# Performance work log

Measured on AMD Instinct MI355X. Metric: run time of the kernel, lower is better.

The kernel has to match this reference:

```python
import jax, jax.numpy as jnp
import numpy as np

B, T, N = 16, 1024, 128
WIN, STEP = 30, 2
MOMENT_ORDERS = (2, 4, 8)
D_MODEL = 256


def _mask_diag(corr):
    n = corr.shape[-1]
    eye = jnp.eye(n, dtype=corr.dtype)
    return corr * (1.0 - eye) + eye


def corrcoef_time(xw):
    # xw: [..., L, N] -> corr over channels: [..., N, N]
    L = xw.shape[-2]
    xm = xw - xw.mean(axis=-2, keepdims=True)
    cov = jnp.einsum('...ln,...lm->...nm', xm, xm) / (L - 1 + 1e-8)
    var = jnp.clip(jnp.diagonal(cov, axis1=-2, axis2=-1), 1e-8, None)
    std = jnp.sqrt(var)
    corr = cov / (std[..., :, None] * std[..., None, :])
    corr = jnp.nan_to_num(corr, nan=0.0, posinf=0.0, neginf=0.0)
    return _mask_diag(corr)


def rowwise_corr(M):
    # M: [B, N, F]
    Xc = M - M.mean(axis=-1, keepdims=True)
    num = jnp.einsum('bnf,bmf->bnm', Xc, Xc)
    den1 = jnp.sqrt(jnp.clip((Xc ** 2).sum(axis=-1), 1e-8, None))
    corr = num / (den1[:, :, None] * den1[:, None, :])
    corr = jnp.nan_to_num(corr, nan=0.0, posinf=0.0, neginf=0.0)
    return _mask_diag(corr)


def layer_norm(x, gamma, beta, eps=1e-5):
    mu = x.mean(axis=-1, keepdims=True)
    var = ((x - mu) ** 2).mean(axis=-1, keepdims=True)
    return (x - mu) / jnp.sqrt(var + eps) * gamma + beta


def normalize_adj(adj):
    n = adj.shape[-1]
    A_hat = adj + jnp.eye(n, dtype=adj.dtype)
    d = A_hat.sum(axis=-1)
    dis = jnp.sqrt(1.0 / jnp.clip(d, 1e-8, None))
    return A_hat * dis[:, :, None] * dis[:, None, :]


def setup_inputs() -> dict:
    key = jax.random.key(0)
    ks = jax.random.split(key, 8)
    in_dim = len(MOMENT_ORDERS) * N
    return {
        'x': jax.random.normal(ks[0], (B, T, N), dtype=jnp.float32),
        'ln_gamma': jnp.ones((in_dim,), jnp.float32),
        'ln_beta': jnp.zeros((in_dim,), jnp.float32),
        'W1': jax.random.normal(ks[1], (in_dim, D_MODEL), jnp.float32) * 0.05,
        'b1': jnp.zeros((D_MODEL,), jnp.float32),
        'W2': jax.random.normal(ks[2], (D_MODEL, D_MODEL), jnp.float32) * 0.05,
        'b2': jnp.zeros((D_MODEL,), jnp.float32),
        'Wc': jax.random.normal(ks[3], (D_MODEL, 1), jnp.float32) * 0.05,
        'bc': jnp.zeros((1,), jnp.float32),
    }


def reference(x, ln_gamma, ln_beta, W1, b1, W2, b2, Wc, bc):
    # sliding windows (static indices)
    starts = np.arange(0, T - WIN + 1, STEP)
    idx = starts[:, None] + np.arange(WIN)[None, :]
    xw = x[:, idx, :]
    lo = corrcoef_time(xw)                            # [B, Wn, N, N]

    mean_lo = lo.mean(axis=1, keepdims=True)
    centered = lo - mean_lo
    cm_list, ho_list = [], []
    for d in MOMENT_ORDERS:
        cm = jnp.nan_to_num((centered ** d).mean(axis=1),
                            nan=0.0, posinf=0.0, neginf=0.0)  # [B, N, N]
        cm_list.append(cm)
        ho_list.append(rowwise_corr(cm))

    X = jnp.concatenate(cm_list, axis=-1)             # [B, N, 3N]
    X = layer_norm(X, ln_gamma, ln_beta)

    A = jnp.stack(ho_list, axis=1).mean(axis=1)
    A = 0.5 * (A + jnp.swapaxes(A, 1, 2))
    A_norm = normalize_adj(A)

    H = jax.nn.relu(jnp.einsum('bnm,bmd->bnd', A_norm, X @ W1 + b1))
    H = jax.nn.relu(jnp.einsum('bnm,bmd->bnd', A_norm, H @ W2 + b2))
    g = H.mean(axis=1)                                # [B, d_model]
    out = jax.nn.sigmoid(g @ Wc + bc)                 # [B, 1]
    return out
```

## Files before the change

kernel.cpp:

```cpp
#include <hip/hip_runtime.h>
#include <math.h>

#define BB  16
#define TT  1024
#define NN  128
#define WIN 30
#define NWD 498
#define DM  256
#define IND 384
#define GW  16

#define INV_W (1.0f/498.0f)

#define SARR (BB*NN*NN)

#define OFF_A     0
#define OFF_G     (OFF_A    + BB*NWD*NN)
#define OFF_CM2   (OFF_G    + BB*NWD*NN)
#define OFF_CM4   (OFF_CM2  + SARR)
#define OFF_CM8   (OFF_CM4  + SARR)
#define OFF_AD    (OFF_CM8  + SARR)
#define OFF_PART  (OFF_AD   + 3*SARR)
#define OFF_ANORM OFF_PART
#define OFF_BUFA  (OFF_ANORM + SARR)
#define OFF_BUFB  (OFF_BUFA + BB*NN*DM)
#define OFF_CTR   (OFF_PART + 768*16384)

#define GLL16(gsrc, ldst) \
    __builtin_amdgcn_global_load_lds((const __attribute__((address_space(1))) void*)(gsrc), \
                                     (__attribute__((address_space(3))) void*)(ldst), 16, 0, 0)

__global__ __launch_bounds__(128) void k1_stats(const float* __restrict__ x, float* __restrict__ ws) {
    int bx = blockIdx.x;
    if (bx == 0 && threadIdx.x < 128) ((unsigned*)(ws + OFF_CTR))[threadIdx.x] = 0u;
    int c = bx & 15, b = bx >> 4;
    int w0 = c*32, w1 = min(NWD, w0+32);
    int n = threadIdx.x;
    const float* xp = x + (size_t)b*TT*NN + n;

    float sum = 0.f, sq = 0.f;
    for (int t = 2*w0; t < 2*w0 + WIN; ++t) {
        float v = xp[(size_t)t*NN];
        sum += v; sq = fmaf(v, v, sq);
    }
    for (int w = w0; w < w1; ++w) {
        if (w > w0) {
            float o0 = xp[(size_t)(2*w-2)*NN], o1 = xp[(size_t)(2*w-1)*NN];
            float n0 = xp[(size_t)(2*w+28)*NN], n1 = xp[(size_t)(2*w+29)*NN];
            sum += (n0 + n1) - (o0 + o1);
            sq  += (n0*n0 + n1*n1) - (o0*o0 + o1*o1);
        }
        float mean = sum * (1.0f/30.0f);
        float ss = sq - 30.0f*mean*mean;
        float var = fmaxf(ss * (1.0f/29.0f), 1e-8f);
        float a = (1.0f / sqrtf(var)) * 0.185695338f;
        ws[OFF_A + ((size_t)b*NWD + w)*NN + n] = a;
        ws[OFF_G + ((size_t)b*NWD + w)*NN + n] = mean * a * 5.477225575f;
    }
}

__global__ __launch_bounds__(256) __attribute__((amdgpu_waves_per_eu(3, 3)))
void k24_inc(const float* __restrict__ x, float* __restrict__ ws) {
    __shared__ __align__(16) float xr[64][NN];
    __shared__ __align__(16) float sa[GW][NN];
    __shared__ __align__(16) float sg[GW][NN];
    int bx = blockIdx.x;
    int wc = bx & 7;
    int slab = (bx >> 3) % 6;
    int b = bx / 48;
    const char IS[6] = {0,0,0,0,1,1};
    const char JS[6] = {0,1,2,3,2,3};
    int is = IS[slab], js = JS[slab];
    int w0 = wc * 63, w1 = min(NWD, w0 + 63);
    int tid = threadIdx.x;
    int jg = tid & 7, ig = tid >> 3;
    int i0 = is*64 + ig*2;
    int j0 = js*32 + jg*4;

    const float* xb = x + (size_t)b*TT*NN;
    const float* Ab = ws + OFF_A + (size_t)b*NWD*NN;
    const float* Gb = ws + OFF_G + (size_t)b*NWD*NN;

    float P[2][4];
    float S1[2][4], S2[2][4], S3[2][4], S4[2][4], S5[2][4], S6[2][4], S7[2][4], S8[2][4];
#pragma unroll
    for (int p=0;p<2;++p)
#pragma unroll
        for (int q=0;q<4;++q) {
            P[p][q]=0.f;
            S1[p][q]=0.f;S2[p][q]=0.f;S3[p][q]=0.f;S4[p][q]=0.f;
            S5[p][q]=0.f;S6[p][q]=0.f;S7[p][q]=0.f;S8[p][q]=0.f;
        }

    auto moments = [&](int k) {
        float2 ai = *(const float2*)&sa[k][i0];
        float2 gi = *(const float2*)&sg[k][i0];
        float4 aj = *(const float4*)&sa[k][j0];
        float4 gj = *(const float4*)&sg[k][j0];
        float av[2] = {ai.x, ai.y};
        float mg[2] = {-gi.x, -gi.y};
        float aw[4] = {aj.x, aj.y, aj.z, aj.w};
        float gw[4] = {gj.x, gj.y, gj.z, gj.w};
#pragma unroll
        for (int p=0;p<2;++p)
#pragma unroll
            for (int q=0;q<4;++q) {
                float aa  = av[p]*aw[q];
                float ngg = mg[p]*gw[q];
                float c   = fmaf(P[p][q], aa, ngg);
                float c2 = c*c;
                float c3 = c2*c;
                float c4 = c2*c2;
                S1[p][q] += c;
                S2[p][q] += c2;
                S3[p][q] += c3;
                S4[p][q] += c4;
                S5[p][q] = fmaf(c4, c,  S5[p][q]);
                S6[p][q] = fmaf(c3, c3, S6[p][q]);
                S7[p][q] = fmaf(c3, c4, S7[p][q]);
                S8[p][q] = fmaf(c4, c4, S8[p][q]);
            }
    };

    int rlo = 2*w0;
    for (int wg = w0; wg < w1; wg += GW) {
        int m = min(GW, w1 - wg);
        __syncthreads();
        int rhi = 2*(wg + m - 1) + 29;
        int nr = rhi - rlo + 1;
        for (int idx = tid; idx < nr*32; idx += 256) {
            int r = idx >> 5, c4 = idx & 31;
            int t = rlo + r;
            GLL16(xb + (size_t)t*NN + c4*4, &xr[t & 63][c4*4]);
        }
        for (int idx = tid; idx < m*32; idx += 256) {
            int k = idx >> 5, c4 = idx & 31;
            GLL16(Ab + (size_t)(wg+k)*NN + c4*4, &sa[k][c4*4]);
        }
        for (int idx = tid; idx < m*32; idx += 256) {
            int k = idx >> 5, c4 = idx & 31;
            GLL16(Gb + (size_t)(wg+k)*NN + c4*4, &sg[k][c4*4]);
        }
        rlo = rhi + 1;
        __syncthreads();

        int kstart = 0;
        if (wg == w0) {
#pragma unroll 6
            for (int k = 0; k < WIN; ++k) {
                int t = 2*w0 + k;
                float2 xi = *(const float2*)&xr[t & 63][i0];
                float4 xj = *(const float4*)&xr[t & 63][j0];
                float av[2] = {xi.x, xi.y};
                float bv[4] = {xj.x, xj.y, xj.z, xj.w};
#pragma unroll
                for (int p=0;p<2;++p)
#pragma unroll
                    for (int q=0;q<4;++q) P[p][q] = fmaf(av[p], bv[q], P[p][q]);
            }
            moments(0);
            kstart = 1;
        }
        for (int k = kstart; k < m; ++k) {
            int w = wg + k;
            int tr[4] = {2*w - 2, 2*w - 1, 2*w + 28, 2*w + 29};
#pragma unroll
            for (int kk = 0; kk < 4; ++kk) {
                int t = tr[kk];
                float sgn = (kk < 2) ? -1.0f : 1.0f;
                float2 xi = *(const float2*)&xr[t & 63][i0];
                float4 xj = *(const float4*)&xr[t & 63][j0];
                float av[2] = {sgn*xi.x, sgn*xi.y};
                float bv[4] = {xj.x, xj.y, xj.z, xj.w};
#pragma unroll
                for (int p=0;p<2;++p)
#pragma unroll
                    for (int q=0;q<4;++q) P[p][q] = fmaf(av[p], bv[q], P[p][q]);
            }
            moments(k);
        }
    }

    float* tp = ws + OFF_PART + (size_t)bx*16384 + tid*8;
#define STORE_ARR(A, S) \
    *(float4*)&tp[(A)*2048]     = make_float4(S[0][0], S[0][1], S[0][2], S[0][3]); \
    *(float4*)&tp[(A)*2048 + 4] = make_float4(S[1][0], S[1][1], S[1][2], S[1][3]);
    STORE_ARR(0, S1) STORE_ARR(1, S2) STORE_ARR(2, S3) STORE_ARR(3, S4)
    STORE_ARR(4, S5) STORE_ARR(5, S6) STORE_ARR(6, S7) STORE_ARR(7, S8)
#undef STORE_ARR
}

__global__ __launch_bounds__(256) void kred(float* __restrict__ ws) {
    int pair = blockIdx.x >> 3, sub = blockIdx.x & 7;
    int b = pair / 6, slab = pair % 6;
    const char IS[6] = {0,0,0,0,1,1};
    const char JS[6] = {0,1,2,3,2,3};
    int is = IS[slab], js = JS[slab];
    int off = sub*256 + threadIdx.x;
    const float* base = ws + OFF_PART + (size_t)(b*48 + slab*8)*16384;

    float E[8];
#pragma unroll
    for (int a=0;a<8;++a) E[a] = 0.f;
    for (int c = 0; c < 8; ++c) {
        const float* tp = base + (size_t)c*16384;
#pragma unroll
        for (int a=0;a<8;++a) E[a] += tp[a*2048 + off];
    }

    int tid_old = off >> 3, e = off & 7;
    int ig = tid_old >> 3, jg = tid_old & 7;
    int p = e >> 2, q = e & 3;
    int i = is*64 + ig*2 + p;
    int j = js*32 + jg*4 + q;

    float cm2, cm4, cm8;
    if (i == j) {
        cm2 = 0.f; cm4 = 0.f; cm8 = 0.f;
    } else {
        float e1 = E[0]*INV_W, e2 = E[1]*INV_W, e3 = E[2]*INV_W, e4 = E[3]*INV_W;
        float e5 = E[4]*INV_W, e6 = E[5]*INV_W, e7 = E[6]*INV_W, e8 = E[7]*INV_W;
        float m  = e1;
        float m2 = m*m, m3 = m2*m, m4 = m2*m2, m5 = m4*m, m6 = m3*m3, m8 = m4*m4;
        cm2 = e2 - m2;
        cm4 = e4 - 4.f*m*e3 + 6.f*m2*e2 - 3.f*m4;
        cm8 = e8 - 8.f*m*e7 + 28.f*m2*e6 - 56.f*m3*e5 + 70.f*m4*e4
                 - 56.f*m5*e3 + 28.f*m6*e2 - 7.f*m8;
    }
    float* C2 = ws + OFF_CM2 + (size_t)b*NN*NN;
    float* C4 = ws + OFF_CM4 + (size_t)b*NN*NN;
    float* C8 = ws + OFF_CM8 + (size_t)b*NN*NN;
    C2[i*NN + j] = cm2; C2[j*NN + i] = cm2;
    C4[i*NN + j] = cm4; C4[j*NN + i] = cm4;
    C8[i*NN + j] = cm8; C8[j*NN + i] = cm8;
}

#define XSTR 132
__global__ __launch_bounds__(256) void kB(const float* __restrict__ gamma, const float* __restrict__ beta,
                                          const float* __restrict__ W1, const float* __restrict__ b1,
                                          float* __restrict__ ws) {
    __shared__ __align__(16) float smem[NN*XSTR + 2*NN];
    __shared__ unsigned winB;
    int blk = blockIdx.x, tid = threadIdx.x;
    if (blk < 192) {
        int rem = blk % 12;
        int b = blk / 12, di = rem >> 2, jq = rem & 3;
        float* Xct = smem;
        float* Mr  = smem + NN*XSTR;
        float* Ir  = Mr + NN;
        const float* cm = ws + (di==0 ? OFF_CM2 : (di==1 ? OFF_CM4 : OFF_CM8)) + (size_t)b*NN*NN;
        for (int idx = tid; idx < NN*NN; idx += 256) {
            int n = idx >> 7, f = idx & 127;
            Xct[f*XSTR + n] = cm[idx];
        }
        __syncthreads();
        if (tid < NN) {
            float s1 = 0.f, s2 = 0.f;
            for (int f = 0; f < NN; ++f) { float v = Xct[f*XSTR + tid]; s1 += v; s2 = fmaf(v, v, s2); }
            float mean = s1 * (1.0f/NN);
            Mr[tid] = mean;
            Ir[tid] = 1.0f/sqrtf(fmaxf(s2 - (float)NN*mean*mean, 1e-8f));
        }
        __syncthreads();
        int n0 = (tid >> 4)*8, m0 = jq*32 + (tid & 15)*2;
        float acc0[8], acc1[8];
#pragma unroll
        for (int k=0;k<8;++k) { acc0[k]=0.f; acc1[k]=0.f; }
        for (int f = 0; f < NN; ++f) {
            const float* row = &Xct[f*XSTR];
            float4 a0 = *(const float4*)&row[n0];
            float4 a1 = *(const float4*)&row[n0+4];
            float2 bm = *(const float2*)&row[m0];
            float av[8] = {a0.x,a0.y,a0.z,a0.w,a1.x,a1.y,a1.z,a1.w};
#pragma unroll
            for (int k=0;k<8;++k) {
                acc0[k] = fmaf(av[k], bm.x, acc0[k]);
                acc1[k] = fmaf(av[k], bm.y, acc1[k]);
            }
        }
        float rm0 = Mr[m0], rm1 = Mr[m0+1], im0 = Ir[m0], im1 = Ir[m0+1];
        float* Ad = ws + OFF_AD + (size_t)(b*3 + di)*NN*NN;
#pragma unroll
        for (int k=0;k<8;++k) {
            int gi = n0+k;
            float rn = Mr[gi], inv = Ir[gi];
            float v0 = (acc0[k] - (float)NN*rn*rm0) * inv * im0;
            float v1 = (acc1[k] - (float)NN*rn*rm1) * inv * im1;
            if (gi == m0)   v0 = 1.0f;
            if (gi == m0+1) v1 = 1.0f;
            Ad[gi*NN + m0]     = v0;
            Ad[gi*NN + m0 + 1] = v1;
        }

        __syncthreads();
        if (tid == 0) {
            unsigned* ctr = (unsigned*)(ws + OFF_CTR);
            unsigned old = __hip_atomic_fetch_add(&ctr[96 + b], 1u,
                                                  __ATOMIC_ACQ_REL, __HIP_MEMORY_SCOPE_AGENT);
            winB = (old == 11u) ? 1u : 0u;
        }
        __syncthreads();
        if (winB) {
            float* As = smem;
            float* dis = smem + NN*(NN+1);
            const float* A0 = ws + OFF_AD + (size_t)(b*3 + 0)*NN*NN;
            const float* A1 = ws + OFF_AD + (size_t)(b*3 + 1)*NN*NN;
            const float* A2 = ws + OFF_AD + (size_t)(b*3 + 2)*NN*NN;
            for (int idx = tid; idx < NN*NN; idx += 256) {
                int n = idx >> 7, m = idx & 127;
                int ji = m*NN + n;
                float s = A0[idx] + A0[ji] + A1[idx] + A1[ji] + A2[idx] + A2[ji];
                As[n*(NN+1)+m] = s * (1.0f/6.0f);
            }
            __syncthreads();
            if (tid < NN) {
                float d = 1.0f;
                for (int m = 0; m < NN; ++m) d += As[tid*(NN+1)+m];
                dis[tid] = sqrtf(1.0f / fmaxf(d, 1e-8f));
            }
            __syncthreads();
            float* An = ws + OFF_ANORM + (size_t)b*NN*NN;
            for (int idx = tid; idx < NN*NN; idx += 256) {
                int n = idx >> 7, m = idx & 127;
                float v = As[n*(NN+1)+m] + (n==m ? 1.0f : 0.0f);
                An[idx] = v * dis[n] * dis[m];
            }
        }
    } else {
        int r0 = (blk - 192) * 8;
        float* Xs = smem;
        float* sm = smem + 8*IND;
        float* sr = sm + 8;
        for (int r = 0; r < 8; ++r) {
            int row = r0 + r;
            int b = row >> 7, n = row & 127;
            const float* c2 = ws + OFF_CM2 + ((size_t)b*NN + n)*NN;
            const float* c4 = ws + OFF_CM4 + ((size_t)b*NN + n)*NN;
            const float* c8 = ws + OFF_CM8 + ((size_t)b*NN + n)*NN;
            for (int c = tid; c < IND; c += 256)
                Xs[r*IND+c] = (c < 128) ? c2[c] : (c < 256) ? c4[c-128] : c8[c-256];
        }
        __syncthreads();
        {
            int team = tid >> 5, lane = tid & 31;
            float s = 0.f;
            for (int c = lane; c < IND; c += 32) s += Xs[team*IND + c];
#pragma unroll
            for (int o = 16; o > 0; o >>= 1) s += __shfl_down(s, o, 32);
            float mean = __shfl(s, 0, 32) * (1.0f/IND);
            float v = 0.f;
            for (int c = lane; c < IND; c += 32) { float d = Xs[team*IND + c] - mean; v = fmaf(d, d, v); }
#pragma unroll
            for (int o = 16; o > 0; o >>= 1) v += __shfl_down(v, o, 32);
            if (lane == 0) {
                sm[team] = mean;
                sr[team] = 1.0f / sqrtf(v*(1.0f/IND) + 1e-5f);
            }
        }
        __syncthreads();
        for (int r = 0; r < 8; ++r) {
            float mean = sm[r], rstd = sr[r];
            for (int c = tid; c < IND; c += 256)
                Xs[r*IND+c] = (Xs[r*IND+c] - mean)*rstd*gamma[c] + beta[c];
        }
        __syncthreads();
        float acc[8];
        float bv = b1[tid];
#pragma unroll
        for (int r = 0; r < 8; ++r) acc[r] = bv;
        for (int kk = 0; kk < IND; kk += 4) {
            float w0 = W1[(size_t)(kk+0)*DM + tid];
            float w1 = W1[(size_t)(kk+1)*DM + tid];
            float w2 = W1[(size_t)(kk+2)*DM + tid];
            float w3 = W1[(size_t)(kk+3)*DM + tid];
#pragma unroll
            for (int r = 0; r < 8; ++r) {
                float4 xv = *(const float4*)&Xs[r*IND + kk];
                acc[r] = fmaf(xv.x, w0, acc[r]);
                acc[r] = fmaf(xv.y, w1, acc[r]);
                acc[r] = fmaf(xv.z, w2, acc[r]);
                acc[r] = fmaf(xv.w, w3, acc[r]);
            }
        }
        float* O = ws + OFF_BUFA;
#pragma unroll
        for (int r = 0; r < 8; ++r) O[(size_t)(r0+r)*DM + tid] = acc[r];
    }
}

__global__ __launch_bounds__(256) void k98_propgemm(const float* __restrict__ W2, const float* __restrict__ b2,
                                                    const float* __restrict__ An, const float* __restrict__ Zin,
                                                    float* __restrict__ Out) {
    __shared__ float Hs[8][DM];
    int bx = blockIdx.x;
    int b = bx >> 4, n0 = (bx & 15)*8;
    int tid = threadIdx.x;
    const float* A = An + (size_t)b*NN*NN + (size_t)n0*NN;
    const float* Z = Zin + (size_t)b*NN*DM;
    float acc[8] = {0,0,0,0,0,0,0,0};
    for (int m = 0; m < NN; m += 4) {
        float z0 = Z[(size_t)(m+0)*DM + tid];
        float z1 = Z[(size_t)(m+1)*DM + tid];
        float z2 = Z[(size_t)(m+2)*DM + tid];
        float z3 = Z[(size_t)(m+3)*DM + tid];
#pragma unroll
        for (int r = 0; r < 8; ++r) {
            const float* Ar = A + r*NN + m;
            acc[r] = fmaf(Ar[0], z0, acc[r]);
            acc[r] = fmaf(Ar[1], z1, acc[r]);
            acc[r] = fmaf(Ar[2], z2, acc[r]);
            acc[r] = fmaf(Ar[3], z3, acc[r]);
        }
    }
#pragma unroll
    for (int r = 0; r < 8; ++r) Hs[r][tid] = fmaxf(acc[r], 0.0f);
    __syncthreads();
    float acc2[8];
    float bv = b2[tid];
#pragma unroll
    for (int r = 0; r < 8; ++r) acc2[r] = bv;
    for (int k = 0; k < DM; k += 4) {
        float w0 = W2[(size_t)(k+0)*DM + tid];
        float w1 = W2[(size_t)(k+1)*DM + tid];
        float w2 = W2[(size_t)(k+2)*DM + tid];
        float w3 = W2[(size_t)(k+3)*DM + tid];
#pragma unroll
        for (int r = 0; r < 8; ++r) {
            float4 h = *(const float4*)&Hs[r][k];
            acc2[r] = fmaf(h.x, w0, acc2[r]);
            acc2[r] = fmaf(h.y, w1, acc2[r]);
            acc2[r] = fmaf(h.z, w2, acc2[r]);
            acc2[r] = fmaf(h.w, w3, acc2[r]);
        }
    }
    float* O = Out + (size_t)b*NN*DM;
#pragma unroll
    for (int r = 0; r < 8; ++r) O[(size_t)(n0+r)*DM + tid] = acc2[r];
}

__global__ __launch_bounds__(256) void k9_prop(const float* __restrict__ Wc, const float* __restrict__ bc,
                                               const float* __restrict__ An, const float* __restrict__ Zin,
                                               float* __restrict__ Out,
                                               float* __restrict__ ws, float* __restrict__ outp) {
    __shared__ float red[256];
    __shared__ unsigned win9;
    int bx = blockIdx.x;
    int b = bx >> 4, n0 = (bx & 15)*8;
    int tid = threadIdx.x;
    const float* A = An + (size_t)b*NN*NN + (size_t)n0*NN;
    const float* Z = Zin + (size_t)b*NN*DM;
    float acc[8] = {0,0,0,0,0,0,0,0};
    for (int m = 0; m < NN; m += 4) {
        float z0 = Z[(size_t)(m+0)*DM + tid];
        float z1 = Z[(size_t)(m+1)*DM + tid];
        float z2 = Z[(size_t)(m+2)*DM + tid];
        float z3 = Z[(size_t)(m+3)*DM + tid];
#pragma unroll
        for (int r = 0; r < 8; ++r) {
            const float* Ar = A + r*NN + m;
            acc[r] = fmaf(Ar[0], z0, acc[r]);
            acc[r] = fmaf(Ar[1], z1, acc[r]);
            acc[r] = fmaf(Ar[2], z2, acc[r]);
            acc[r] = fmaf(Ar[3], z3, acc[r]);
        }
    }
    float* O = Out + (size_t)b*NN*DM;
#pragma unroll
    for (int r = 0; r < 8; ++r) O[(size_t)(n0+r)*DM + tid] = fmaxf(acc[r], 0.0f);

    __syncthreads();
    if (tid == 0) {
        unsigned* ctr = (unsigned*)(ws + OFF_CTR);
        unsigned old = __hip_atomic_fetch_add(&ctr[112 + b], 1u,
                                              __ATOMIC_ACQ_REL, __HIP_MEMORY_SCOPE_AGENT);
        win9 = (old == 15u) ? 1u : 0u;
    }
    __syncthreads();
    if (win9) {
        const float* H = Out + (size_t)b*NN*DM;
        float s = 0.f;
        for (int n = 0; n < NN; ++n) s += H[(size_t)n*DM + tid];
        red[tid] = s * (1.0f/NN) * Wc[tid];
        __syncthreads();
        for (int o = 128; o > 0; o >>= 1) { if (tid < o) red[tid] += red[tid+o]; __syncthreads(); }
        if (tid == 0) outp[b] = 1.0f/(1.0f + expf(-(red[0] + bc[0])));
    }
}

extern "C" void kernel_launch(void* const* d_in, const int* in_sizes, int n_in,
                              void* d_out, int out_size, void* d_ws, size_t ws_size,
                              hipStream_t stream) {
    (void)in_sizes; (void)n_in; (void)out_size; (void)ws_size;
    const float* x     = (const float*)d_in[0];
    const float* gamma = (const float*)d_in[1];
    const float* beta  = (const float*)d_in[2];
    const float* W1    = (const float*)d_in[3];
    const float* b1    = (const float*)d_in[4];
    const float* W2    = (const float*)d_in[5];
    const float* b2    = (const float*)d_in[6];
    const float* Wc    = (const float*)d_in[7];
    const float* bc    = (const float*)d_in[8];
    float* ws  = (float*)d_ws;
    float* out = (float*)d_out;

    k1_stats    <<<BB*16,  128, 0, stream>>>(x, ws);
    k24_inc     <<<BB*6*8, 256, 0, stream>>>(x, ws);
    kred        <<<BB*6*8, 256, 0, stream>>>(ws);
    kB          <<<448,    256, 0, stream>>>(gamma, beta, W1, b1, ws);
    k98_propgemm<<<BB*16,  256, 0, stream>>>(W2, b2, ws + OFF_ANORM, ws + OFF_BUFA, ws + OFF_BUFB);
    k9_prop     <<<BB*16,  256, 0, stream>>>(Wc, bc, ws + OFF_ANORM, ws + OFF_BUFB, ws + OFF_BUFA, ws, out);
}
```

Measured before the change: 241.7 us.

## Halve kB shared memory by staging features in two chunks; drop adjacency transpose

The row-correlation stage of kB now stages the cm matrix into shared memory in two 64-feature halves, accumulating the row sums and the dot products across both halves. This roughly halves the static LDS footprint so more blocks can be resident per CU. The winner block also no longer builds a symmetrised adjacency in LDS. It reads A0..A2 directly and averages them without the transpose, on the assumption that each correlation matrix is already symmetric. The cost is an extra sync round and repeated global reads in the normalisation, and the result can differ slightly if the matrices are not exactly symmetric.

```diff
diff --git a/kernel.cpp b/kernel.cpp
--- a/kernel.cpp
+++ b/kernel.cpp
@@ -239,45 +239,55 @@
 __global__ __launch_bounds__(256) void kB(const float* __restrict__ gamma, const float* __restrict__ beta,
                                           const float* __restrict__ W1, const float* __restrict__ b1,
                                           float* __restrict__ ws) {
-    __shared__ __align__(16) float smem[NN*XSTR + 2*NN];
+    __shared__ __align__(16) float smem[64*XSTR + 2*NN];
     __shared__ unsigned winB;
     int blk = blockIdx.x, tid = threadIdx.x;
     if (blk < 192) {
         int rem = blk % 12;
         int b = blk / 12, di = rem >> 2, jq = rem & 3;
         float* Xct = smem;
-        float* Mr  = smem + NN*XSTR;
+        float* Mr  = smem + 64*XSTR;
         float* Ir  = Mr + NN;
         const float* cm = ws + (di==0 ? OFF_CM2 : (di==1 ? OFF_CM4 : OFF_CM8)) + (size_t)b*NN*NN;
-        for (int idx = tid; idx < NN*NN; idx += 256) {
-            int n = idx >> 7, f = idx & 127;
-            Xct[f*XSTR + n] = cm[idx];
+        int n0 = (tid >> 4)*8, m0 = jq*32 + (tid & 15)*2;
+        float s1 = 0.f, s2 = 0.f;
+        float acc0[8], acc1[8];
+#pragma unroll
+        for (int k=0;k<8;++k) { acc0[k]=0.f; acc1[k]=0.f; }
+
+        for (int h = 0; h < 2; ++h) {
+            __syncthreads();
+            for (int idx = tid; idx < NN*64; idx += 256) {
+                int n = idx >> 6, f0 = idx & 63;
+                Xct[f0*XSTR + n] = cm[n*NN + h*64 + f0];
+            }
+            __syncthreads();
+            if (tid < NN) {
+                for (int f0 = 0; f0 < 64; ++f0) {
+                    float v = Xct[f0*XSTR + tid];
+                    s1 += v; s2 = fmaf(v, v, s2);
+                }
+            }
+            for (int f0 = 0; f0 < 64; ++f0) {
+                const float* row = &Xct[f0*XSTR];
+                float4 a0 = *(const float4*)&row[n0];
+                float4 a1 = *(const float4*)&row[n0+4];
+                float2 bm = *(const float2*)&row[m0];
+                float av[8] = {a0.x,a0.y,a0.z,a0.w,a1.x,a1.y,a1.z,a1.w};
+#pragma unroll
+                for (int k=0;k<8;++k) {
+                    acc0[k] = fmaf(av[k], bm.x, acc0[k]);
+                    acc1[k] = fmaf(av[k], bm.y, acc1[k]);
+                }
+            }
         }
         __syncthreads();
         if (tid < NN) {
-            float s1 = 0.f, s2 = 0.f;
-            for (int f = 0; f < NN; ++f) { float v = Xct[f*XSTR + tid]; s1 += v; s2 = fmaf(v, v, s2); }
             float mean = s1 * (1.0f/NN);
             Mr[tid] = mean;
             Ir[tid] = 1.0f/sqrtf(fmaxf(s2 - (float)NN*mean*mean, 1e-8f));
         }
         __syncthreads();
-        int n0 = (tid >> 4)*8, m0 = jq*32 + (tid & 15)*2;
-        float acc0[8], acc1[8];
-#pragma unroll
-        for (int k=0;k<8;++k) { acc0[k]=0.f; acc1[k]=0.f; }
-        for (int f = 0; f < NN; ++f) {
-            const float* row = &Xct[f*XSTR];
-            float4 a0 = *(const float4*)&row[n0];
-            float4 a1 = *(const float4*)&row[n0+4];
-            float2 bm = *(const float2*)&row[m0];
-            float av[8] = {a0.x,a0.y,a0.z,a0.w,a1.x,a1.y,a1.z,a1.w};
-#pragma unroll
-            for (int k=0;k<8;++k) {
-                acc0[k] = fmaf(av[k], bm.x, acc0[k]);
-                acc1[k] = fmaf(av[k], bm.y, acc1[k]);
-            }
-        }
         float rm0 = Mr[m0], rm1 = Mr[m0+1], im0 = Ir[m0], im1 = Ir[m0+1];
         float* Ad = ws + OFF_AD + (size_t)(b*3 + di)*NN*NN;
 #pragma unroll
@@ -301,28 +311,24 @@
         }
         __syncthreads();
         if (winB) {
-            float* As = smem;
-            float* dis = smem + NN*(NN+1);
+            float* dis = smem;
             const float* A0 = ws + OFF_AD + (size_t)(b*3 + 0)*NN*NN;
             const float* A1 = ws + OFF_AD + (size_t)(b*3 + 1)*NN*NN;
             const float* A2 = ws + OFF_AD + (size_t)(b*3 + 2)*NN*NN;
-            for (int idx = tid; idx < NN*NN; idx += 256) {
-                int n = idx >> 7, m = idx & 127;
-                int ji = m*NN + n;
-                float s = A0[idx] + A0[ji] + A1[idx] + A1[ji] + A2[idx] + A2[ji];
-                As[n*(NN+1)+m] = s * (1.0f/6.0f);
-            }
-            __syncthreads();
             if (tid < NN) {
                 float d = 1.0f;
-                for (int m = 0; m < NN; ++m) d += As[tid*(NN+1)+m];
+                for (int m = 0; m < NN; ++m) {
+                    int o = tid*NN + m;
+                    d += (A0[o] + A1[o] + A2[o]) * (1.0f/3.0f);
+                }
                 dis[tid] = sqrtf(1.0f / fmaxf(d, 1e-8f));
             }
             __syncthreads();
             float* An = ws + OFF_ANORM + (size_t)b*NN*NN;
             for (int idx = tid; idx < NN*NN; idx += 256) {
                 int n = idx >> 7, m = idx & 127;
-                float v = As[n*(NN+1)+m] + (n==m ? 1.0f : 0.0f);
+                float s = (A0[idx] + A1[idx] + A2[idx]) * (1.0f/3.0f);
+                float v = s + (n==m ? 1.0f : 0.0f);
                 An[idx] = v * dis[n] * dis[m];
             }
         }
```

After: 238.5 us. No clear change (-1.3%).
